# Kernel optimization log

Measured on AMD Instinct MI355X. Metric: run time of the kernel, lower is better.

The kernel has to match this reference:

```python
import jax, jax.numpy as jnp
import numpy as np

C, H, W, P = 3, 32, 32, 16
Z = P * P  # 256
B, S = 128, 1024
EPS = 1e-06
MAX_VAL, MIN_VAL = 5.0, -5.0


def setup_inputs() -> dict:
    key = jax.random.key(0)
    ks = jax.random.split(key, 8)
    patches = jax.random.normal(ks[0], (B, S, Z), dtype=jnp.float32)
    pos_channels = jax.random.randint(ks[1], (B, S), 0, C)
    pos_h = jax.random.randint(ks[2], (B, S), 0, H)
    pos_w = jax.random.randint(ks[3], (B, S), 0, W)
    key_pad_mask = jax.random.randint(ks[4], (B, S), 0, 2).astype(bool)
    # running Welford stats buffers (simulate partially-trained state)
    n = 100.0 * jax.random.uniform(ks[5], (C, H, W), dtype=jnp.float32)
    mean = jax.random.normal(ks[6], (C, H, W, Z), dtype=jnp.float32)
    m2 = 10.0 * jax.random.uniform(ks[7], (C, H, W, Z), dtype=jnp.float32)
    return {"patches": patches, "pos_channels": pos_channels, "pos_h": pos_h,
            "pos_w": pos_w, "key_pad_mask": key_pad_mask, "n": n, "mean": mean, "m2": m2}


def _patchnorm(patches, pos_channels, pos_h, pos_w, key_pad_mask, n, mean, m2):
    # Flatten token dims; padded tokens are masked (contribute 0) instead of
    # boolean-compressed, keeping shapes static under jit.
    N = B * S
    p = patches.reshape(N, Z)
    valid = (~key_pad_mask).reshape(N).astype(p.dtype)  # [N]
    flat = (pos_channels * (H * W) + pos_h * W + pos_w).reshape(N)  # [N]

    n_flat = n.reshape(C * H * W)
    mean_flat = mean.reshape(C * H * W, Z)
    m2_flat = m2.reshape(C * H * W, Z)

    # --- Welford batched update (matches torch scatter_add_3d sequence) ---
    n_new = n_flat.at[flat].add(valid)                         # n += 1 per valid token
    delta = p - mean_flat[flat]                                # gather old mean
    contrib = (delta * valid[:, None]) / jnp.maximum(n_new[flat], 1.0)[:, None]
    mean_new = mean_flat.at[flat].add(contrib)                 # mean += delta/n
    delta2 = p - mean_new[flat]                                # gather new mean
    m2_new = m2_flat.at[flat].add(delta * delta2 * valid[:, None])

    # --- variance / std (var=1 where n<2) ---
    var = m2_new / jnp.maximum(n_new, 1.0)[:, None]
    var = jnp.where((n_new < 2.0)[:, None], 1.0, var)
    std = jnp.sqrt(var)

    # --- normalize with updated stats, clamp, zero out padding ---
    normed = (p - mean_new[flat]) / (std[flat] + EPS)
    normed = jnp.clip(normed, MIN_VAL, MAX_VAL) * valid[:, None]
    return normed.reshape(B, S, Z)


def reference(patches, pos_channels, pos_h, pos_w, key_pad_mask, n, mean, m2):
    return _patchnorm(patches, pos_channels, pos_h, pos_w, key_pad_mask, n, mean, m2)
```

## Files before the change

### kernel.cpp

```cpp
#include <hip/hip_runtime.h>

#define CC 3
#define HH 32
#define WW 32
#define ZZ 256
#define NCELL (CC*HH*WW)
#define NTOK  (128*1024)
#define CAP   128
#define EPSV  1e-6f
#define VBIT  (1 << 30)


__global__ __launch_bounds__(256) void build_kernel(
        const int* __restrict__ pc, const int* __restrict__ ph,
        const int* __restrict__ pw, const int* __restrict__ mask,
        int* __restrict__ cursor, int* __restrict__ list) {
    int t = blockIdx.x * blockDim.x + threadIdx.x;
    if (t >= NTOK) return;
    int cell  = pc[t] * (HH * WW) + ph[t] * WW + pw[t];
    int valid = (mask[t] == 0) ? VBIT : 0;
    int slot  = atomicAdd(&cursor[cell], 1);
    if (slot < CAP) list[cell * CAP + slot] = t | valid;
}

__global__ __launch_bounds__(64) void cell_kernel(
        const float4* __restrict__ patch4, const float* __restrict__ nbuf,
        const float4* __restrict__ mean4,  const float4* __restrict__ m24,
        const int* __restrict__ cursor,    const int* __restrict__ list,
        float4* __restrict__ out4) {
    __shared__ int slist[CAP];
    const int c    = blockIdx.x;
    const int lane = threadIdx.x;

    int cnt = cursor[c];
    if (cnt > CAP) cnt = CAP;

    int e0 = 0, e1 = 0;
    if (lane < cnt)      { e0 = list[c * CAP + lane];      slist[lane]      = e0; }
    if (lane + 64 < cnt) { e1 = list[c * CAP + lane + 64]; slist[lane + 64] = e1; }

    unsigned long long b0 = __ballot((lane < cnt)      && (e0 & VBIT));
    unsigned long long b1 = __ballot((lane + 64 < cnt) && (e1 & VBIT));
    const float cv = (float)(__popcll(b0) + __popcll(b1));

    const float n_new = nbuf[c] + cv;
    const float denom = fmaxf(n_new, 1.0f);
    const float4 m_old = mean4[c * 64 + lane];

    float sq0 = 0.f, sq1 = 0.f, sq2 = 0.f, sq3 = 0.f;
    float ss0 = 0.f, ss1 = 0.f, ss2 = 0.f, ss3 = 0.f;
    for (int i = 0; i < cnt; ++i) {
        int e = slist[i];
        if (e & VBIT) {
            int t = e & 0x3FFFFFFF;
            float4 p = patch4[t * 64 + lane];
            float q0 = p.x - m_old.x, q1 = p.y - m_old.y;
            float q2 = p.z - m_old.z, q3 = p.w - m_old.w;
            sq0 += q0; sq1 += q1; sq2 += q2; sq3 += q3;
            ss0 += q0 * q0; ss1 += q1 * q1; ss2 += q2 * q2; ss3 += q3 * q3;
        }
    }

    const float4 m2v = m24[c * 64 + lane];
    const float dm0 = sq0 / denom, dm1 = sq1 / denom;
    const float dm2 = sq2 / denom, dm3 = sq3 / denom;
    const float mn0 = m_old.x + dm0, mn1 = m_old.y + dm1;
    const float mn2 = m_old.z + dm2, mn3 = m_old.w + dm3;
    const bool small_n = (n_new < 2.0f);
    float v0 = small_n ? 1.0f : ((m2v.x + (ss0 - dm0 * sq0)) / denom);
    float v1 = small_n ? 1.0f : ((m2v.y + (ss1 - dm1 * sq1)) / denom);
    float v2 = small_n ? 1.0f : ((m2v.z + (ss2 - dm2 * sq2)) / denom);
    float v3 = small_n ? 1.0f : ((m2v.w + (ss3 - dm3 * sq3)) / denom);
    const float i0 = 1.0f / (sqrtf(v0) + EPSV);
    const float i1 = 1.0f / (sqrtf(v1) + EPSV);
    const float i2 = 1.0f / (sqrtf(v2) + EPSV);
    const float i3 = 1.0f / (sqrtf(v3) + EPSV);

    for (int i = 0; i < cnt; ++i) {
        int e = slist[i];
        int t = e & 0x3FFFFFFF;
        float4 o = make_float4(0.f, 0.f, 0.f, 0.f);
        if (e & VBIT) {
            float4 p = patch4[t * 64 + lane];
            o.x = fminf(fmaxf((p.x - mn0) * i0, -5.0f), 5.0f);
            o.y = fminf(fmaxf((p.y - mn1) * i1, -5.0f), 5.0f);
            o.z = fminf(fmaxf((p.z - mn2) * i2, -5.0f), 5.0f);
            o.w = fminf(fmaxf((p.w - mn3) * i3, -5.0f), 5.0f);
        }
        out4[t * 64 + lane] = o;
    }
}

extern "C" void kernel_launch(void* const* d_in, const int* in_sizes, int n_in,
                              void* d_out, int out_size, void* d_ws, size_t ws_size,
                              hipStream_t stream) {
    const float* patches = (const float*)d_in[0];
    const int*   pc      = (const int*)  d_in[1];
    const int*   ph      = (const int*)  d_in[2];
    const int*   pw      = (const int*)  d_in[3];
    const int*   mask    = (const int*)  d_in[4];
    const float* nbuf    = (const float*)d_in[5];
    const float* mean    = (const float*)d_in[6];
    const float* m2      = (const float*)d_in[7];
    float*       out     = (float*)d_out;

    int* cursor = (int*)d_ws;
    int* list   = cursor + NCELL;

    hipMemsetAsync(cursor, 0, NCELL * sizeof(int), stream);

    build_kernel<<<(NTOK + 255) / 256, 256, 0, stream>>>(
        pc, ph, pw, mask, cursor, list);

    cell_kernel<<<NCELL, 64, 0, stream>>>(
        (const float4*)patches, nbuf, (const float4*)mean, (const float4*)m2,
        cursor, list, (float4*)out);
}
```

Before: 271.9 us.

## Replace global-atomic bucketing with histogram-scan counting sort and two-wave cell blocks

```diff
diff --git a/kernel.cpp b/kernel.cpp
--- a/kernel.cpp
+++ b/kernel.cpp
@@ -6,50 +6,129 @@
 #define ZZ 256
 #define NCELL (CC*HH*WW)
 #define NTOK  (128*1024)
-#define CAP   128
+#define NB    128
+#define TPB_TOK 1024
+#define LCAP  256
 #define EPSV  1e-6f
 #define VBIT  (1 << 30)
 
 
-__global__ __launch_bounds__(256) void build_kernel(
+
+__global__ __launch_bounds__(256) void hist_kernel(
+        const int* __restrict__ pc, const int* __restrict__ ph,
+        const int* __restrict__ pw, int* __restrict__ H) {
+    __shared__ int h[NCELL];
+    for (int i = threadIdx.x; i < NCELL; i += 256) h[i] = 0;
+    __syncthreads();
+    const int t0 = blockIdx.x * TPB_TOK;
+    for (int k = 0; k < TPB_TOK; k += 256) {
+        int t = t0 + k + threadIdx.x;
+        int cell = pc[t] * (HH * WW) + ph[t] * WW + pw[t];
+        atomicAdd(&h[cell], 1);
+    }
+    __syncthreads();
+    for (int i = threadIdx.x; i < NCELL; i += 256)
+        H[blockIdx.x * NCELL + i] = h[i];
+}
+
+__global__ __launch_bounds__(256) void sum_kernel(
+        const int* __restrict__ H, int* __restrict__ cnt) {
+    int c = blockIdx.x * 256 + threadIdx.x;
+    int s = 0;
+    for (int b = 0; b < NB; ++b) s += H[b * NCELL + c];
+    cnt[c] = s;
+}
+
+__global__ __launch_bounds__(256) void scan_kernel(
+        const int* __restrict__ cnt, int* __restrict__ base) {
+    __shared__ int tot[256];
+    const int t = threadIdx.x;
+    int loc[12]; int s = 0;
+    for (int j = 0; j < 12; ++j) { loc[j] = s; s += cnt[t * 12 + j]; }
+    tot[t] = s;
+    __syncthreads();
+    for (int off = 1; off < 256; off <<= 1) {
+        int v = tot[t];
+        int u = (t >= off) ? tot[t - off] : 0;
+        __syncthreads();
+        tot[t] = v + u;
+        __syncthreads();
+    }
+    const int excl = tot[t] - s;
+    for (int j = 0; j < 12; ++j) base[t * 12 + j] = excl + loc[j];
+}
+
+__global__ __launch_bounds__(256) void offset_kernel(
+        int* __restrict__ H, const int* __restrict__ base) {
+    int c = blockIdx.x * 256 + threadIdx.x;
+    int run = base[c];
+    for (int b = 0; b < NB; ++b) {
+        int idx = b * NCELL + c;
+        int h = H[idx];
+        H[idx] = run;
+        run += h;
+    }
+}
+
+__global__ __launch_bounds__(256) void scatter_kernel(
         const int* __restrict__ pc, const int* __restrict__ ph,
         const int* __restrict__ pw, const int* __restrict__ mask,
-        int* __restrict__ cursor, int* __restrict__ list) {
-    int t = blockIdx.x * blockDim.x + threadIdx.x;
-    if (t >= NTOK) return;
-    int cell  = pc[t] * (HH * WW) + ph[t] * WW + pw[t];
-    int valid = (mask[t] == 0) ? VBIT : 0;
-    int slot  = atomicAdd(&cursor[cell], 1);
-    if (slot < CAP) list[cell * CAP + slot] = t | valid;
-}
-
-__global__ __launch_bounds__(64) void cell_kernel(
+        const int* __restrict__ Hs, int* __restrict__ list) {
+    __shared__ int rank[NCELL];
+    __shared__ int sbase[NCELL];
+    for (int i = threadIdx.x; i < NCELL; i += 256) {
+        rank[i] = 0;
+        sbase[i] = Hs[blockIdx.x * NCELL + i];
+    }
+    __syncthreads();
+    const int t0 = blockIdx.x * TPB_TOK;
+    for (int k = 0; k < TPB_TOK; k += 256) {
+        int t = t0 + k + threadIdx.x;
+        int cell = pc[t] * (HH * WW) + ph[t] * WW + pw[t];
+        int r = atomicAdd(&rank[cell], 1);
+        int valid = (mask[t] == 0) ? VBIT : 0;
+        list[sbase[cell] + r] = t | valid;
+    }
+}
+
+
+__global__ __launch_bounds__(128) void cell_kernel(
         const float4* __restrict__ patch4, const float* __restrict__ nbuf,
         const float4* __restrict__ mean4,  const float4* __restrict__ m24,
-        const int* __restrict__ cursor,    const int* __restrict__ list,
-        float4* __restrict__ out4) {
-    __shared__ int slist[CAP];
+        const int* __restrict__ cnt_,      const int* __restrict__ base_,
+        const int* __restrict__ list,      float4* __restrict__ out4) {
+    __shared__ int   slist[LCAP];
+    __shared__ float part[8][128];
+    __shared__ int   cvs;
     const int c    = blockIdx.x;
-    const int lane = threadIdx.x;
-
-    int cnt = cursor[c];
-    if (cnt > CAP) cnt = CAP;
-
-    int e0 = 0, e1 = 0;
-    if (lane < cnt)      { e0 = list[c * CAP + lane];      slist[lane]      = e0; }
-    if (lane + 64 < cnt) { e1 = list[c * CAP + lane + 64]; slist[lane + 64] = e1; }
-
-    unsigned long long b0 = __ballot((lane < cnt)      && (e0 & VBIT));
-    unsigned long long b1 = __ballot((lane + 64 < cnt) && (e1 & VBIT));
-    const float cv = (float)(__popcll(b0) + __popcll(b1));
-
+    const int tid  = threadIdx.x;
+    const int wave = tid >> 6;
+    const int lane = tid & 63;
+
+    int cnt = cnt_[c];
+    if (cnt > LCAP) cnt = LCAP;
+    const int base = base_[c];
+
+    if (tid == 0) cvs = 0;
+    __syncthreads();
+
+    int myv = 0;
+    for (int i = tid; i < cnt; i += 128) {
+        int e = list[base + i];
+        slist[i] = e;
+        myv += (e >> 30) & 1;
+    }
+    if (myv) atomicAdd(&cvs, myv);
+    __syncthreads();
+
+    const float cv    = (float)cvs;
     const float n_new = nbuf[c] + cv;
     const float denom = fmaxf(n_new, 1.0f);
     const float4 m_old = mean4[c * 64 + lane];
 
     float sq0 = 0.f, sq1 = 0.f, sq2 = 0.f, sq3 = 0.f;
     float ss0 = 0.f, ss1 = 0.f, ss2 = 0.f, ss3 = 0.f;
-    for (int i = 0; i < cnt; ++i) {
+    for (int i = wave; i < cnt; i += 2) {
         int e = slist[i];
         if (e & VBIT) {
             int t = e & 0x3FFFFFFF;
@@ -60,23 +139,35 @@
             ss0 += q0 * q0; ss1 += q1 * q1; ss2 += q2 * q2; ss3 += q3 * q3;
         }
     }
+    part[0][tid] = sq0; part[1][tid] = sq1; part[2][tid] = sq2; part[3][tid] = sq3;
+    part[4][tid] = ss0; part[5][tid] = ss1; part[6][tid] = ss2; part[7][tid] = ss3;
+    __syncthreads();
+
+    const float Sq0 = part[0][lane] + part[0][64 + lane];
+    const float Sq1 = part[1][lane] + part[1][64 + lane];
+    const float Sq2 = part[2][lane] + part[2][64 + lane];
+    const float Sq3 = part[3][lane] + part[3][64 + lane];
+    const float Ss0 = part[4][lane] + part[4][64 + lane];
+    const float Ss1 = part[5][lane] + part[5][64 + lane];
+    const float Ss2 = part[6][lane] + part[6][64 + lane];
+    const float Ss3 = part[7][lane] + part[7][64 + lane];
 
     const float4 m2v = m24[c * 64 + lane];
-    const float dm0 = sq0 / denom, dm1 = sq1 / denom;
-    const float dm2 = sq2 / denom, dm3 = sq3 / denom;
+    const float dm0 = Sq0 / denom, dm1 = Sq1 / denom;
+    const float dm2 = Sq2 / denom, dm3 = Sq3 / denom;
     const float mn0 = m_old.x + dm0, mn1 = m_old.y + dm1;
     const float mn2 = m_old.z + dm2, mn3 = m_old.w + dm3;
     const bool small_n = (n_new < 2.0f);
-    float v0 = small_n ? 1.0f : ((m2v.x + (ss0 - dm0 * sq0)) / denom);
-    float v1 = small_n ? 1.0f : ((m2v.y + (ss1 - dm1 * sq1)) / denom);
-    float v2 = small_n ? 1.0f : ((m2v.z + (ss2 - dm2 * sq2)) / denom);
-    float v3 = small_n ? 1.0f : ((m2v.w + (ss3 - dm3 * sq3)) / denom);
+    float v0 = small_n ? 1.0f : ((m2v.x + (Ss0 - dm0 * Sq0)) / denom);
+    float v1 = small_n ? 1.0f : ((m2v.y + (Ss1 - dm1 * Sq1)) / denom);
+    float v2 = small_n ? 1.0f : ((m2v.z + (Ss2 - dm2 * Sq2)) / denom);
+    float v3 = small_n ? 1.0f : ((m2v.w + (Ss3 - dm3 * Sq3)) / denom);
     const float i0 = 1.0f / (sqrtf(v0) + EPSV);
     const float i1 = 1.0f / (sqrtf(v1) + EPSV);
     const float i2 = 1.0f / (sqrtf(v2) + EPSV);
     const float i3 = 1.0f / (sqrtf(v3) + EPSV);
 
-    for (int i = 0; i < cnt; ++i) {
+    for (int i = wave; i < cnt; i += 2) {
         int e = slist[i];
         int t = e & 0x3FFFFFFF;
         float4 o = make_float4(0.f, 0.f, 0.f, 0.f);
@@ -104,15 +195,18 @@
     const float* m2      = (const float*)d_in[7];
     float*       out     = (float*)d_out;
 
-    int* cursor = (int*)d_ws;
-    int* list   = cursor + NCELL;
-
-    hipMemsetAsync(cursor, 0, NCELL * sizeof(int), stream);
-
-    build_kernel<<<(NTOK + 255) / 256, 256, 0, stream>>>(
-        pc, ph, pw, mask, cursor, list);
-
-    cell_kernel<<<NCELL, 64, 0, stream>>>(
+    int* H    = (int*)d_ws;
+    int* cnt  = H + NB * NCELL;
+    int* base = cnt + NCELL;
+    int* list = base + NCELL;
+
+    hist_kernel   <<<NB,          256, 0, stream>>>(pc, ph, pw, H);
+    sum_kernel    <<<NCELL / 256, 256, 0, stream>>>(H, cnt);
+    scan_kernel   <<<1,           256, 0, stream>>>(cnt, base);
+    offset_kernel <<<NCELL / 256, 256, 0, stream>>>(H, base);
+    scatter_kernel<<<NB,          256, 0, stream>>>(pc, ph, pw, mask, H, list);
+
+    cell_kernel<<<NCELL, 128, 0, stream>>>(
         (const float4*)patches, nbuf, (const float4*)mean, (const float4*)m2,
-        cursor, list, (float4*)out);
-}
+        cnt, base, list, (float4*)out);
+}
```

After: 272.5 us. About the same (+0.2%).
